# Kernel optimization log

Measured on AMD Instinct MI355X. Metric: run time of the kernel, lower is better.

The kernel has to match this reference:

```python
import jax, jax.numpy as jnp
import numpy as np

H = 16  # num heads

def setup_inputs() -> dict:
    key = jax.random.key(0)
    ks = jax.random.split(key, 5)
    B, T, E = 4, 2048, 1024
    return {
        "x": jax.random.normal(ks[0], (B, T, E), dtype=jnp.float32),
        "in_proj_weight": jax.random.normal(ks[1], (3 * E, E), dtype=jnp.float32) * (1.0 / np.sqrt(E)),
        "in_proj_bias": jax.random.normal(ks[2], (3 * E,), dtype=jnp.float32) * 0.02,
        "out_w": jax.random.normal(ks[3], (E, E), dtype=jnp.float32) * (1.0 / np.sqrt(E)),
        "out_b": jax.random.normal(ks[4], (E,), dtype=jnp.float32) * 0.02,
    }


def reference(x, in_proj_weight, in_proj_bias, out_w, out_b):
    B, T, E = x.shape
    D = E // H
    scale = D ** -0.5
    wq, wk, wv = jnp.split(in_proj_weight, 3, axis=0)  # each [E, E]
    bq, bk, bv = jnp.split(in_proj_bias, 3, axis=0)
    # projections (self-attention: q=k=v source)
    q = (x @ wq.T + bq) * scale            # [B, T, E]
    k = x @ wk.T + bk
    v = x @ wv.T + bv
    # split heads -> [B, H, T, D]
    def heads(t):
        return t.reshape(B, T, H, D).transpose(0, 2, 1, 3)
    q, k, v = heads(q), heads(k), heads(v)
    scores = jnp.einsum('bhqd,bhkd->bhqk', q, k)       # [B, H, T, T]
    probs = jax.nn.softmax(scores, axis=-1)
    attn = jnp.einsum('bhqk,bhkd->bhqd', probs, v)     # [B, H, T, D]
    attn = attn.transpose(0, 2, 1, 3).reshape(B, T, E)
    out = attn @ out_w.T + out_b                       # out_proj (nn.Linear)
    return (out, probs / scale)
```

## Files before the change

kernel.cpp:

```cpp
#include <hip/hip_runtime.h>


#define DEV __device__ __forceinline__

typedef __attribute__((ext_vector_type(8))) short short8;
typedef __attribute__((ext_vector_type(4))) float f32x4;

DEV unsigned short f2b(float f) {
  union { float f; unsigned u; } v; v.f = f;
  unsigned r = v.u + 0x7fffu + ((v.u >> 16) & 1u);
  return (unsigned short)(r >> 16);
}
DEV unsigned pk2(float lo, float hi) {
  return (unsigned)f2b(lo) | ((unsigned)f2b(hi) << 16);
}
#if __has_builtin(__builtin_amdgcn_exp2f)
DEV float exp2_fast(float x) { return __builtin_amdgcn_exp2f(x); }
#else
DEV float exp2_fast(float x) { return exp2f(x); }
#endif
DEV void gl_lds16(const void* g, void* l) {
  __builtin_amdgcn_global_load_lds(
      (const __attribute__((address_space(1))) void*)g,
      (__attribute__((address_space(3))) void*)l, 16, 0, 0);
}
DEV void bar_lgkm() { asm volatile("s_waitcnt lgkmcnt(0)\n\ts_barrier" ::: "memory"); }

__global__ void cvt_f32_bf16(const float* __restrict__ src, unsigned short* __restrict__ dst, int n) {
  int i = (blockIdx.x * blockDim.x + threadIdx.x) * 4;
  if (i >= n) return;
  float4 v = *(const float4*)(src + i);
  ushort4 o; o.x = f2b(v.x); o.y = f2b(v.y); o.z = f2b(v.z); o.w = f2b(v.w);
  *(ushort4*)(dst + i) = o;
}

template<int MODE>
__global__ __launch_bounds__(256, 2) void gemm_bt(
    const unsigned short* __restrict__ A,
    const unsigned short* __restrict__ B,
    const float* __restrict__ bias,
    float* __restrict__ Cf,
    unsigned short* __restrict__ Cqk,
    unsigned short* __restrict__ Vtg,
    int N, int K)
{
  constexpr int BK = 64;
  __shared__ __align__(16) unsigned short As[128*BK];
  __shared__ __align__(16) unsigned short Bs[128*BK];
  const int tid = threadIdx.x, lane = tid & 63, wid = tid >> 6;
  const int lhi = lane >> 4, llo = lane & 15;
  const int m0 = blockIdx.y * 128, n0 = blockIdx.x * 128;
  const int wr = wid >> 1, wc = wid & 1;

  f32x4 acc[4][4] = {};

  const int nsteps = K / BK;
  for (int kt = 0; kt < nsteps; ++kt) {
    __syncthreads();
#pragma unroll
    for (int s = 0; s < 4; ++s) {
      int u = wid*4 + s;
      int a = u*1024 + lane*16;
      int t = a >> 7;
      int cb = (a & 127) ^ ((t & 7) << 4);
      int e = kt*BK + (cb >> 1);
      gl_lds16(A + (size_t)(m0 + t)*K + e, (char*)As + u*1024);
      gl_lds16(B + (size_t)(n0 + t)*K + e, (char*)Bs + u*1024);
    }
    __syncthreads();
#pragma unroll
    for (int kk = 0; kk < 2; ++kk) {
      short8 af[4], bfr[4];
#pragma unroll
      for (int mf = 0; mf < 4; ++mf) {
        int row = wr*64 + mf*16 + llo;
        af[mf] = *(const short8*)((const char*)As + row*128 + ((kk*64 + lhi*16) ^ ((row & 7) << 4)));
      }
#pragma unroll
      for (int nf = 0; nf < 4; ++nf) {
        int row = wc*64 + nf*16 + llo;
        bfr[nf] = *(const short8*)((const char*)Bs + row*128 + ((kk*64 + lhi*16) ^ ((row & 7) << 4)));
      }
#pragma unroll
      for (int mf = 0; mf < 4; ++mf)
#pragma unroll
        for (int nf = 0; nf < 4; ++nf)
          acc[mf][nf] = __builtin_amdgcn_mfma_f32_16x16x32_bf16(af[mf], bfr[nf], acc[mf][nf], 0, 0, 0);
    }
  }
  if (MODE == 0) {
#pragma unroll
    for (int mf = 0; mf < 4; ++mf)
#pragma unroll
      for (int nf = 0; nf < 4; ++nf) {
        int n = n0 + wc*64 + nf*16 + llo;
        float bv = bias[n];
#pragma unroll
        for (int r = 0; r < 4; ++r) {
          int m = m0 + wr*64 + mf*16 + lhi*4 + r;
          __builtin_nontemporal_store(acc[mf][nf][r] + bv, &Cf[(size_t)m*N + n]);
        }
      }
  } else {
    if (n0 < 2048) {
#pragma unroll
      for (int mf = 0; mf < 4; ++mf)
#pragma unroll
        for (int nf = 0; nf < 4; ++nf) {
          int n = n0 + wc*64 + nf*16 + llo;
          float bv = bias[n];
          float sc = (n < 1024) ? 0.125f * 1.44269504088896f : 1.0f;
#pragma unroll
          for (int r = 0; r < 4; ++r) {
            int m = m0 + wr*64 + mf*16 + lhi*4 + r;
            Cqk[(size_t)m*2048 + n] = f2b((acc[mf][nf][r] + bv) * sc);
          }
        }
    } else {
#pragma unroll
      for (int mf = 0; mf < 4; ++mf)
#pragma unroll
        for (int nf = 0; nf < 4; ++nf) {
          int n = n0 + wc*64 + nf*16 + llo;
          float bv = bias[n];
          int hh = (n - 2048) >> 6, d = (n - 2048) & 63;
          int m = m0 + wr*64 + mf*16 + lhi*4;
          int bb = m >> 11, t = m & 2047;
          ushort4 o;
          o.x = f2b(acc[mf][nf][0] + bv);
          o.y = f2b(acc[mf][nf][1] + bv);
          o.z = f2b(acc[mf][nf][2] + bv);
          o.w = f2b(acc[mf][nf][3] + bv);
          *(ushort4*)(Vtg + ((size_t)((bb << 4) + hh)*64 + d)*2048 + t) = o;
        }
    }
  }
}

__global__ __launch_bounds__(256, 3) void mha_fused(
    const unsigned short* __restrict__ qk,
    const unsigned short* __restrict__ vtg,
    float* __restrict__ probs,
    unsigned short* __restrict__ attnb)
{
  constexpr int T = 2048, LD = 2048, QB = 64, TB = 128, NT = T / TB;
  __shared__ __align__(16) unsigned short Kslot[TB*64];
  __shared__ __align__(16) unsigned short Vslot[64*TB];
  __shared__ __align__(16) unsigned short Ps[QB*TB];
  __shared__ float lsum[4][QB];
  __shared__ float linv[QB];

  const int tid = threadIdx.x, lane = tid & 63, wid = tid >> 6;
  const int lhi = lane >> 4, llo = lane & 15;
  const int wg = ((blockIdx.x & 7) << 8) | (blockIdx.x >> 3);
  const int qt = wg & 31, bh = wg >> 5;
  const int bb = bh >> 4, h = bh & 15;
  const int q0 = qt * QB;
  const size_t tokQ = (size_t)bb*T + q0;

  auto stageK = [&](int tt, unsigned short* buf) {
#pragma unroll
    for (int s = 0; s < 4; ++s) {
      int u = wid*4 + s;
      int a = u*1024 + lane*16;
      int tr = a >> 7;
      int cb = (a & 127) ^ ((tr & 7) << 4);
      gl_lds16(qk + ((size_t)bb*T + tt*TB + tr)*LD + 1024 + h*64 + (cb >> 1),
               (char*)buf + u*1024);
    }
  };
  auto stageV = [&](int tt) {
#pragma unroll
    for (int s = 0; s < 4; ++s) {
      int u = wid*4 + s;
      int a = u*1024 + lane*16;
      int d = a >> 8;
      int cb = (a & 255) ^ ((d & 7) << 4);
      gl_lds16(vtg + ((size_t)bh*64 + d)*T + tt*TB + (cb >> 1),
               (char*)Vslot + u*1024);
    }
  };
  auto bsel = [&](int m) -> unsigned short* {
    return (m == 0) ? Kslot : ((m == 1) ? Vslot : Ps);
  };

#pragma unroll
  for (int s = 0; s < 2; ++s) {
    int u = wid*2 + s;
    int a = u*1024 + lane*16;
    int tr = a >> 7;
    int cb = (a & 127) ^ ((tr & 7) << 4);
    gl_lds16(qk + (tokQ + tr)*LD + h*64 + (cb >> 1), (char*)Ps + u*1024);
  }
  stageK(0, Kslot);
  stageK(1, Vslot);
  asm volatile("s_waitcnt vmcnt(8)" ::: "memory");
  __builtin_amdgcn_s_barrier();

  short8 qfr[4][2];
#pragma unroll
  for (int qf = 0; qf < 4; ++qf)
#pragma unroll
    for (int kk = 0; kk < 2; ++kk) {
      int row = qf*16 + llo;
      qfr[qf][kk] = *(const short8*)((const char*)Ps + row*128 + ((kk*64 + lhi*16) ^ ((row & 7) << 4)));
    }
  bar_lgkm();

  float part[4] = {0.f, 0.f, 0.f, 0.f};
  int m3 = 0;
  int s3 = 2;
  for (int tt = 0; tt < NT; ++tt) {
    if (tt + 2 < NT) stageK(tt + 2, bsel(s3));
    if (tt + 2 < NT)      asm volatile("s_waitcnt vmcnt(8)" ::: "memory");
    else if (tt + 1 < NT) asm volatile("s_waitcnt vmcnt(4)" ::: "memory");
    else                  asm volatile("s_waitcnt vmcnt(0)" ::: "memory");
    const unsigned short* cur = bsel(m3);
    f32x4 sacc[2][4] = {};
#pragma unroll
    for (int kk = 0; kk < 2; ++kk) {
      short8 kf[2];
#pragma unroll
      for (int tf = 0; tf < 2; ++tf) {
        int row = wid*32 + tf*16 + llo;
        kf[tf] = *(const short8*)((const char*)cur + row*128 + ((kk*64 + lhi*16) ^ ((row & 7) << 4)));
      }
#pragma unroll
      for (int tf = 0; tf < 2; ++tf)
#pragma unroll
        for (int qf = 0; qf < 4; ++qf)
          sacc[tf][qf] = __builtin_amdgcn_mfma_f32_16x16x32_bf16(kf[tf], qfr[qf][kk], sacc[tf][qf], 0, 0, 0);
    }
#pragma unroll
    for (int tf = 0; tf < 2; ++tf)
#pragma unroll
      for (int qf = 0; qf < 4; ++qf)
#pragma unroll
        for (int r = 0; r < 4; ++r)
          part[qf] += exp2_fast(sacc[tf][qf][r]);
    m3 = (m3 + 1 == 3) ? 0 : m3 + 1;
    s3 = (s3 + 1 == 3) ? 0 : s3 + 1;
  }

#pragma unroll
  for (int qf = 0; qf < 4; ++qf) {
    float v = part[qf];
    v += __shfl_xor(v, 16);
    v += __shfl_xor(v, 32);
    if (lhi == 0) lsum[wid][qf*16 + llo] = v;
  }
  bar_lgkm();
  if (tid < QB) linv[tid] = 1.0f / (lsum[0][tid] + lsum[1][tid] + lsum[2][tid] + lsum[3][tid]);
  stageK(0, Kslot);
  stageV(0);
  bar_lgkm();
  float lr[4];
#pragma unroll
  for (int qf = 0; qf < 4; ++qf) lr[qf] = linv[qf*16 + llo];

  f32x4 pv[4] = {};
  for (int tt = 0; tt < NT; ++tt) {
    if (tt == 0) asm volatile("s_waitcnt vmcnt(4)"  ::: "memory");
    else         asm volatile("s_waitcnt vmcnt(12)" ::: "memory");
    f32x4 sacc[2][4] = {};
#pragma unroll
    for (int kk = 0; kk < 2; ++kk) {
      short8 kf[2];
#pragma unroll
      for (int tf = 0; tf < 2; ++tf) {
        int row = wid*32 + tf*16 + llo;
        kf[tf] = *(const short8*)((const char*)Kslot + row*128 + ((kk*64 + lhi*16) ^ ((row & 7) << 4)));
      }
#pragma unroll
      for (int tf = 0; tf < 2; ++tf)
#pragma unroll
        for (int qf = 0; qf < 4; ++qf)
          sacc[tf][qf] = __builtin_amdgcn_mfma_f32_16x16x32_bf16(kf[tf], qfr[qf][kk], sacc[tf][qf], 0, 0, 0);
    }
    asm volatile("s_waitcnt lgkmcnt(0)" ::: "memory");
    __builtin_amdgcn_sched_barrier(0);
    stageK((tt + 1) & 15, Kslot);
#pragma unroll
    for (int tf = 0; tf < 2; ++tf)
#pragma unroll
      for (int qf = 0; qf < 4; ++qf) {
        float p0 = exp2_fast(sacc[tf][qf][0]) * lr[qf];
        float p1 = exp2_fast(sacc[tf][qf][1]) * lr[qf];
        float p2 = exp2_fast(sacc[tf][qf][2]) * lr[qf];
        float p3 = exp2_fast(sacc[tf][qf][3]) * lr[qf];
        int q = qf*16 + llo;
        int t0 = wid*32 + tf*16 + lhi*4;
        uint2 w2; w2.x = pk2(p0, p1); w2.y = pk2(p2, p3);
        *(uint2*)((char*)Ps + q*256 + ((t0*2) ^ ((q & 7) << 4))) = w2;
        f32x4 pv4; pv4[0] = 8.f*p0; pv4[1] = 8.f*p1; pv4[2] = 8.f*p2; pv4[3] = 8.f*p3;
        __builtin_nontemporal_store(pv4,
            (f32x4*)&probs[((size_t)bh*T + q0 + q)*T + tt*TB + t0]);
      }
    asm volatile("s_waitcnt vmcnt(12) lgkmcnt(0)\n\ts_barrier" ::: "memory");
#pragma unroll
    for (int kk2 = 0; kk2 < 4; ++kk2) {
      int rq = wid*16 + llo;
      short8 pb = *(const short8*)((const char*)Ps + rq*256 + ((kk2*64 + lhi*16) ^ ((rq & 7) << 4)));
#pragma unroll
      for (int mf = 0; mf < 4; ++mf) {
        int rd = mf*16 + llo;
        short8 va = *(const short8*)((const char*)Vslot + rd*256 + ((kk2*64 + lhi*16) ^ ((rd & 7) << 4)));
        pv[mf] = __builtin_amdgcn_mfma_f32_16x16x32_bf16(va, pb, pv[mf], 0, 0, 0);
      }
    }
    asm volatile("s_waitcnt lgkmcnt(0)\n\ts_barrier" ::: "memory");
    stageV((tt + 1) & 15);
  }

#pragma unroll
  for (int mf = 0; mf < 4; ++mf) {
    int q = wid*16 + llo;
    int d0 = mf*16 + lhi*4;
    ushort4 o;
    o.x = f2b(pv[mf][0]); o.y = f2b(pv[mf][1]);
    o.z = f2b(pv[mf][2]); o.w = f2b(pv[mf][3]);
    *(ushort4*)(attnb + (tokQ + q)*1024 + h*64 + d0) = o;
  }
}

extern "C" void kernel_launch(void* const* d_in, const int* in_sizes, int n_in,
                              void* d_out, int out_size, void* d_ws, size_t ws_size,
                              hipStream_t stream) {
  (void)in_sizes; (void)n_in; (void)out_size; (void)ws_size;
  const float* x    = (const float*)d_in[0];
  const float* wqkv = (const float*)d_in[1];
  const float* bqkv = (const float*)d_in[2];
  const float* wout = (const float*)d_in[3];
  const float* bout = (const float*)d_in[4];

  constexpr int T = 2048, E = 1024;
  constexpr int M = 4 * T;
  constexpr size_t NX   = (size_t)M * E;
  constexpr size_t NW1  = (size_t)3 * E * E;
  constexpr size_t NW2  = (size_t)E * E;
  constexpr size_t NQK  = (size_t)M * 2048;
  constexpr size_t NVT  = (size_t)64 * 64 * T;

  char* ws = (char*)d_ws;
  unsigned short* xb    = (unsigned short*)ws;  ws += NX  * 2;
  unsigned short* wqkvb = (unsigned short*)ws;  ws += NW1 * 2;
  unsigned short* woutb = (unsigned short*)ws;  ws += NW2 * 2;
  unsigned short* qkb   = (unsigned short*)ws;  ws += NQK * 2;
  unsigned short* vtg   = (unsigned short*)ws;  ws += NVT * 2;
  unsigned short* attnb = (unsigned short*)ws;  ws += NX  * 2;

  cvt_f32_bf16<<<(int)(NX  / 1024), 256, 0, stream>>>(x,    xb,    (int)NX);
  cvt_f32_bf16<<<(int)(NW1 / 1024), 256, 0, stream>>>(wqkv, wqkvb, (int)NW1);
  cvt_f32_bf16<<<(int)(NW2 / 1024), 256, 0, stream>>>(wout, woutb, (int)NW2);

  gemm_bt<1><<<dim3(3*E/128, M/128), 256, 0, stream>>>(
      xb, wqkvb, bqkv, nullptr, qkb, vtg, 3*E, E);

  float* probsOut = (float*)d_out + NX;
  mha_fused<<<4*16*(T/64), 256, 0, stream>>>(qkb, vtg, probsOut, attnb);

  gemm_bt<0><<<dim3(E/128, M/128), 256, 0, stream>>>(
      attnb, woutb, bout, (float*)d_out, nullptr, nullptr, E, E);
}
```

Baseline: 367.3 us.

## Split PV over key slices per wave to remove per-tile barriers, reduce at end

In the second attention pass, each wave now computes P·V only for its own 32-key slice across all 64 queries, using wave-private P and V LDS regions. Because no wave reads another wave's data inside the loop, the two s_barriers per key tile go away. The cost is a 4x larger PV accumulator (64 extra VGPRs) and a final cross-wave reduction through LDS. That raises register pressure and could lower occupancy.

```diff
diff --git a/kernel.cpp b/kernel.cpp
--- a/kernel.cpp
+++ b/kernel.cpp
@@ -172,12 +172,11 @@
   auto stageV = [&](int tt) {
 #pragma unroll
     for (int s = 0; s < 4; ++s) {
-      int u = wid*4 + s;
-      int a = u*1024 + lane*16;
-      int d = a >> 8;
-      int cb = (a & 255) ^ ((d & 7) << 4);
-      gl_lds16(vtg + ((size_t)bh*64 + d)*T + tt*TB + (cb >> 1),
-               (char*)Vslot + u*1024);
+      int a = s*1024 + lane*16;
+      int d = a >> 6;
+      int tb = (a & 63) ^ ((d & 3) << 4);
+      gl_lds16(vtg + ((size_t)bh*64 + d)*T + tt*TB + wid*32 + (tb >> 1),
+               (char*)Vslot + wid*4096 + s*1024);
     }
   };
   auto bsel = [&](int m) -> unsigned short* {
@@ -208,8 +207,7 @@
   bar_lgkm();
 
   float part[4] = {0.f, 0.f, 0.f, 0.f};
-  int m3 = 0;
-  int s3 = 2;
+  int m3 = 0, s3 = 2;
   for (int tt = 0; tt < NT; ++tt) {
     if (tt + 2 < NT) stageK(tt + 2, bsel(s3));
     if (tt + 2 < NT)      asm volatile("s_waitcnt vmcnt(8)" ::: "memory");
@@ -258,58 +256,87 @@
 #pragma unroll
   for (int qf = 0; qf < 4; ++qf) lr[qf] = linv[qf*16 + llo];
 
-  f32x4 pv[4] = {};
+  f32x4 pv[4][4] = {};
   for (int tt = 0; tt < NT; ++tt) {
-    if (tt == 0) asm volatile("s_waitcnt vmcnt(4)"  ::: "memory");
-    else         asm volatile("s_waitcnt vmcnt(12)" ::: "memory");
-    f32x4 sacc[2][4] = {};
-#pragma unroll
-    for (int kk = 0; kk < 2; ++kk) {
-      short8 kf[2];
-#pragma unroll
-      for (int tf = 0; tf < 2; ++tf) {
+    asm volatile("s_waitcnt vmcnt(4)" ::: "memory");
+#pragma unroll
+    for (int tf = 0; tf < 2; ++tf) {
+      f32x4 s4[4] = {};
+#pragma unroll
+      for (int kk = 0; kk < 2; ++kk) {
         int row = wid*32 + tf*16 + llo;
-        kf[tf] = *(const short8*)((const char*)Kslot + row*128 + ((kk*64 + lhi*16) ^ ((row & 7) << 4)));
-      }
-#pragma unroll
-      for (int tf = 0; tf < 2; ++tf)
+        short8 kf = *(const short8*)((const char*)Kslot + row*128 + ((kk*64 + lhi*16) ^ ((row & 7) << 4)));
 #pragma unroll
         for (int qf = 0; qf < 4; ++qf)
-          sacc[tf][qf] = __builtin_amdgcn_mfma_f32_16x16x32_bf16(kf[tf], qfr[qf][kk], sacc[tf][qf], 0, 0, 0);
+          s4[qf] = __builtin_amdgcn_mfma_f32_16x16x32_bf16(kf, qfr[qf][kk], s4[qf], 0, 0, 0);
+      }
+#pragma unroll
+      for (int qf = 0; qf < 4; ++qf) {
+        float p0 = exp2_fast(s4[qf][0]) * lr[qf];
+        float p1 = exp2_fast(s4[qf][1]) * lr[qf];
+        float p2 = exp2_fast(s4[qf][2]) * lr[qf];
+        float p3 = exp2_fast(s4[qf][3]) * lr[qf];
+        int q = qf*16 + llo;
+        uint2 w2; w2.x = pk2(p0, p1); w2.y = pk2(p2, p3);
+        *(uint2*)((char*)Ps + wid*4096 + q*64 + ((tf*32 + lhi*8) ^ ((q & 3) << 4))) = w2;
+        int t0 = wid*32 + tf*16 + lhi*4;
+        f32x4 pv4; pv4[0] = 8.f*p0; pv4[1] = 8.f*p1; pv4[2] = 8.f*p2; pv4[3] = 8.f*p3;
+        __builtin_nontemporal_store(pv4,
+            (f32x4*)&probs[((size_t)bh*T + q0 + q)*T + tt*TB + t0]);
+      }
     }
     asm volatile("s_waitcnt lgkmcnt(0)" ::: "memory");
     __builtin_amdgcn_sched_barrier(0);
     stageK((tt + 1) & 15, Kslot);
-#pragma unroll
-    for (int tf = 0; tf < 2; ++tf)
-#pragma unroll
-      for (int qf = 0; qf < 4; ++qf) {
-        float p0 = exp2_fast(sacc[tf][qf][0]) * lr[qf];
-        float p1 = exp2_fast(sacc[tf][qf][1]) * lr[qf];
-        float p2 = exp2_fast(sacc[tf][qf][2]) * lr[qf];
-        float p3 = exp2_fast(sacc[tf][qf][3]) * lr[qf];
-        int q = qf*16 + llo;
-        int t0 = wid*32 + tf*16 + lhi*4;
-        uint2 w2; w2.x = pk2(p0, p1); w2.y = pk2(p2, p3);
-        *(uint2*)((char*)Ps + q*256 + ((t0*2) ^ ((q & 7) << 4))) = w2;
-        f32x4 pv4; pv4[0] = 8.f*p0; pv4[1] = 8.f*p1; pv4[2] = 8.f*p2; pv4[3] = 8.f*p3;
-        __builtin_nontemporal_store(pv4,
-            (f32x4*)&probs[((size_t)bh*T + q0 + q)*T + tt*TB + t0]);
-      }
-    asm volatile("s_waitcnt vmcnt(12) lgkmcnt(0)\n\ts_barrier" ::: "memory");
-#pragma unroll
-    for (int kk2 = 0; kk2 < 4; ++kk2) {
-      int rq = wid*16 + llo;
-      short8 pb = *(const short8*)((const char*)Ps + rq*256 + ((kk2*64 + lhi*16) ^ ((rq & 7) << 4)));
+    asm volatile("s_waitcnt vmcnt(12)" ::: "memory");
+    __builtin_amdgcn_sched_barrier(0);
+#pragma unroll
+    for (int qb = 0; qb < 4; ++qb) {
+      int rq = qb*16 + llo;
+      short8 pb = *(const short8*)((const char*)Ps + wid*4096 + rq*64 + ((lhi*16) ^ ((rq & 3) << 4)));
 #pragma unroll
       for (int mf = 0; mf < 4; ++mf) {
         int rd = mf*16 + llo;
-        short8 va = *(const short8*)((const char*)Vslot + rd*256 + ((kk2*64 + lhi*16) ^ ((rd & 7) << 4)));
-        pv[mf] = __builtin_amdgcn_mfma_f32_16x16x32_bf16(va, pb, pv[mf], 0, 0, 0);
-      }
-    }
-    asm volatile("s_waitcnt lgkmcnt(0)\n\ts_barrier" ::: "memory");
+        short8 va = *(const short8*)((const char*)Vslot + wid*4096 + rd*64 + ((lhi*16) ^ ((rd & 3) << 4)));
+        pv[mf][qb] = __builtin_amdgcn_mfma_f32_16x16x32_bf16(va, pb, pv[mf][qb], 0, 0, 0);
+      }
+    }
+    asm volatile("s_waitcnt lgkmcnt(0)" ::: "memory");
+    __builtin_amdgcn_sched_barrier(0);
     stageV((tt + 1) & 15);
+  }
+
+  asm volatile("s_waitcnt vmcnt(0) lgkmcnt(0)\n\ts_barrier" ::: "memory");
+  auto redbase = [&](int region) -> char* {
+    return ((region < 4) ? (char*)Kslot : (region < 8) ? (char*)Vslot : (char*)Ps)
+           + (region & 3)*4096;
+  };
+#pragma unroll
+  for (int qb = 0; qb < 4; ++qb) {
+    if (qb != wid) {
+      int j = (wid < qb) ? wid : wid - 1;
+      char* base = redbase(qb*3 + j) + (lhi*16 + llo)*16;
+#pragma unroll
+      for (int mf = 0; mf < 4; ++mf)
+        *(f32x4*)(base + mf*1024) = pv[mf][qb];
+    }
+  }
+  asm volatile("s_waitcnt lgkmcnt(0)\n\ts_barrier" ::: "memory");
+  f32x4 own[4] = {};
+#pragma unroll
+  for (int qb = 0; qb < 4; ++qb)
+    if (qb == wid)
+#pragma unroll
+      for (int mf = 0; mf < 4; ++mf) own[mf] = pv[mf][qb];
+#pragma unroll
+  for (int j = 0; j < 3; ++j) {
+    char* base = redbase(wid*3 + j) + (lhi*16 + llo)*16;
+#pragma unroll
+    for (int mf = 0; mf < 4; ++mf) {
+      f32x4 t4 = *(const f32x4*)(base + mf*1024);
+#pragma unroll
+      for (int r = 0; r < 4; ++r) own[mf][r] += t4[r];
+    }
   }
 
 #pragma unroll
@@ -317,8 +344,8 @@
     int q = wid*16 + llo;
     int d0 = mf*16 + lhi*4;
     ushort4 o;
-    o.x = f2b(pv[mf][0]); o.y = f2b(pv[mf][1]);
-    o.z = f2b(pv[mf][2]); o.w = f2b(pv[mf][3]);
+    o.x = f2b(own[mf][0]); o.y = f2b(own[mf][1]);
+    o.z = f2b(own[mf][2]); o.w = f2b(own[mf][3]);
     *(ushort4*)(attnb + (tokQ + q)*1024 + h*64 + d0) = o;
   }
 }
```

Result: slower. 385.2 us (+4.9%).
